# Kernel tuning notes

Hardware: AMD Instinct MI355X
Metric: run time of the kernel (lower is better)

The kernel has to match this reference:

```python
import jax, jax.numpy as jnp
import numpy as np

FACTOR = 5  # sampling factor c

def setup_inputs() -> dict:
    key = jax.random.key(0)
    k1, k2, k3, k4 = jax.random.split(key, 4)
    B, H, L, D = 4, 8, 2048, 64
    u = min(max(1, FACTOR * int(np.ceil(np.log(L)))), L)  # sample_k = 40
    return {
        "queries": jax.random.normal(k1, (B, H, L, D), jnp.float32),
        "keys": jax.random.normal(k2, (B, H, L, D), jnp.float32),
        "values": jax.random.normal(k3, (B, H, L, D), jnp.float32),
        "index_sample": jax.random.randint(k4, (L, u), 0, L, jnp.int32),
    }

def reference(queries, keys, values, index_sample):
    B, H, L_Q, D = queries.shape
    L_K = keys.shape[2]
    scale = 1.0 / np.sqrt(D)
    U_part = min(max(1, FACTOR * int(np.ceil(np.log(L_K)))), L_Q)  # n_top queries

    # --- _prob_QK: sampled scores + sparsity measure ---
    # K_sample[b,h,q,s,:] = keys[b,h,index_sample[q,s],:]  -> (B,H,L_Q,u,D)
    K_sample = keys[:, :, index_sample, :]
    QK_sample = jnp.einsum('bhqd,bhqsd->bhqs', queries, K_sample)  # (B,H,L_Q,u)
    M = QK_sample.max(-1) - QK_sample.sum(-1) / L_K                # (B,H,L_Q)
    _, index = jax.lax.top_k(M, U_part)                            # (B,H,U)

    # --- initial context: mean of V for non-selected queries ---
    context = jnp.broadcast_to(values.mean(-2, keepdims=True), (B, H, L_Q, D))

    # --- full attention for the top-U queries only ---
    Q_reduce = jnp.take_along_axis(queries, index[..., None], axis=2)   # (B,H,U,D)
    scores = jnp.einsum('bhud,bhkd->bhuk', Q_reduce, keys) * scale      # (B,H,U,L_K)
    attn = jax.nn.softmax(scores, axis=-1)
    out = jnp.einsum('bhuk,bhkd->bhud', attn, values)                   # (B,H,U,D)

    # --- scatter selected outputs back into the mean context ---
    bi = jnp.arange(B)[:, None, None]
    hi = jnp.arange(H)[None, :, None]
    context = context.at[bi, hi, index].set(out)
    return context
```

## Files before the change

### kernel.cpp

```cpp
#include <hip/hip_runtime.h>
#include <math.h>

#define Bq 4
#define Hh 8
#define Lh 2048
#define Dh 64
#define BH (Bq*Hh)

__global__ __launch_bounds__(256) void kAC(const float* __restrict__ Q,
                                           const float* __restrict__ K,
                                           const float* __restrict__ V,
                                           const int* __restrict__ idxs,
                                           float2* __restrict__ M2,
                                           float* __restrict__ vpart, int u) {
    int bi = blockIdx.x;
    int tid = threadIdx.x;
    if (bi < 2048) {
        int xcd = bi & 7, slot = bi >> 3;
        int bh  = xcd * 4 + (slot >> 6);
        int qt  = (slot >> 1) & 31;
        int half = slot & 1;
        int wave = tid >> 6, lane = tid & 63;
        int g = lane >> 2, c = lane & 3;
        int q = qt * 64 + wave * 16 + g;
        long gq = (long)bh * Lh + q;

        const float* qrow = Q + gq * Dh;
        float4 qf[4];
#pragma unroll
        for (int jj = 0; jj < 4; ++jj)
            qf[jj] = *(const float4*)(qrow + jj * 16 + c * 4);

        int cnt1 = u >> 1;
        int c0 = (half == 0) ? (u - cnt1) : cnt1;
        const int* irow = idxs + (long)q * u + (half ? (u - cnt1) : 0);
        const float* kbase = K + (long)bh * Lh * Dh;

        float mx = -INFINITY, sm = 0.f;
        int s = 0;
        for (; s + 4 <= c0; s += 4) {
            int i0 = irow[s], i1 = irow[s+1], i2 = irow[s+2], i3 = irow[s+3];
            const float* kp0 = kbase + (long)i0 * Dh + c * 4;
            const float* kp1 = kbase + (long)i1 * Dh + c * 4;
            const float* kp2 = kbase + (long)i2 * Dh + c * 4;
            const float* kp3 = kbase + (long)i3 * Dh + c * 4;
            float4 kf[4][4];
#pragma unroll
            for (int jj = 0; jj < 4; ++jj) {
                kf[0][jj] = *(const float4*)(kp0 + jj * 16);
                kf[1][jj] = *(const float4*)(kp1 + jj * 16);
                kf[2][jj] = *(const float4*)(kp2 + jj * 16);
                kf[3][jj] = *(const float4*)(kp3 + jj * 16);
            }
            float a[4];
#pragma unroll
            for (int r = 0; r < 4; ++r) {
                float ac = 0.f;
#pragma unroll
                for (int jj = 0; jj < 4; ++jj)
                    ac += qf[jj].x*kf[r][jj].x + qf[jj].y*kf[r][jj].y
                        + qf[jj].z*kf[r][jj].z + qf[jj].w*kf[r][jj].w;
                a[r] = ac;
            }
#pragma unroll
            for (int r = 0; r < 4; ++r) {
                a[r] += __shfl_xor(a[r], 1);
                a[r] += __shfl_xor(a[r], 2);
                mx = fmaxf(mx, a[r]); sm += a[r];
            }
        }
        for (; s < c0; ++s) {
            int ki = irow[s];
            const float* krow = kbase + (long)ki * Dh + c * 4;
            float acc = 0.f;
#pragma unroll
            for (int jj = 0; jj < 4; ++jj) {
                float4 kf = *(const float4*)(krow + jj * 16);
                acc += qf[jj].x*kf.x + qf[jj].y*kf.y + qf[jj].z*kf.z + qf[jj].w*kf.w;
            }
            acc += __shfl_xor(acc, 1);
            acc += __shfl_xor(acc, 2);
            mx = fmaxf(mx, acc); sm += acc;
        }
        if (c == 0) M2[gq * 2 + half] = make_float2(mx, sm);
    } else {
        int b2 = bi - 2048;
        int xcd = b2 & 7, slot = b2 >> 3;
        int bh = xcd * 4 + (slot >> 3);
        int chunk = slot & 7;
        int d = tid & 63, r0 = tid >> 6;
        const float* vb = V + ((long)bh * Lh + chunk * 256) * Dh;
        float s = 0.f;
        for (int i = 0; i < 64; ++i) s += vb[(r0 + 4 * i) * Dh + d];
        __shared__ float part[4][64];
        part[r0][d] = s;
        __syncthreads();
        if (tid < 64) {
            float t = part[0][tid] + part[1][tid] + part[2][tid] + part[3][tid];
            vpart[(bh * 8 + chunk) * 64 + tid] = t;
        }
    }
}

__global__ __launch_bounds__(256) void kBE(const float2* __restrict__ M2,
                                           const float* __restrict__ vpart,
                                           int* __restrict__ topk,
                                           float* __restrict__ ctx, int U) {
    int bi = blockIdx.x;
    int tid = threadIdx.x;
    if (bi < 4096) {
        long base = (long)bi * 1024;
        int bh = (int)(base >> 17);
        __shared__ float vm[64];
        if (tid < 64) {
            float s = 0.f;
#pragma unroll
            for (int c2 = 0; c2 < 8; ++c2) s += vpart[(bh * 8 + c2) * 64 + tid];
            vm[tid] = s * (1.0f / (float)Lh);
        }
        __syncthreads();
        float4 val = *(const float4*)(vm + ((tid * 4) & 63));
        *(float4*)(ctx + base + tid * 4) = val;
        return;
    }
    int bh = bi - 4096;
    unsigned key[8];
#pragma unroll
    for (int j = 0; j < 8; ++j) {
        long q = (long)bh * Lh + tid + 256 * j;
        float4 mm = *(const float4*)(&M2[q * 2]);
        float Mv = fmaxf(mm.x, mm.z) - (mm.y + mm.w) * (1.0f / (float)Lh);
        unsigned ub = __float_as_uint(Mv);
        key[j] = ub ^ ((ub >> 31) ? 0xFFFFFFFFu : 0x80000000u);
    }
    __shared__ unsigned hist[256];
    __shared__ unsigned prefix_s;
    __shared__ int need_s;
    if (tid == 0) { prefix_s = 0u; need_s = U; }

    for (int level = 3; level >= 0; --level) {
        int shift = level * 8;
        hist[tid] = 0u;
        __syncthreads();
        unsigned prefix = prefix_s;
        int need = need_s;
        unsigned pmask = (level == 3) ? 0u : (0xFFFFFFFFu << (shift + 8));
#pragma unroll
        for (int j = 0; j < 8; ++j)
            if ((key[j] & pmask) == prefix)
                atomicAdd(&hist[(key[j] >> shift) & 0xFF], 1u);
        __syncthreads();
        if (tid < 64) {
            int lane = tid;
            unsigned h0 = hist[lane*4+0], h1 = hist[lane*4+1],
                     h2 = hist[lane*4+2], h3 = hist[lane*4+3];
            unsigned lt = h0 + h1 + h2 + h3;
            unsigned ssum = lt;
#pragma unroll
            for (int off = 1; off < 64; off <<= 1) {
                unsigned t = __shfl_down(ssum, off);
                if (lane + off < 64) ssum += t;
            }
            unsigned sx  = ssum - lt;
            unsigned suf3 = sx  + h3;
            unsigned suf2 = suf3 + h2;
            unsigned suf1 = suf2 + h1;
            unsigned suf0 = suf1 + h0;
            int localb = -1; unsigned nxt = 0u;
            if      ((int)suf3 >= need) { localb = lane*4+3; nxt = sx;   }
            else if ((int)suf2 >= need) { localb = lane*4+2; nxt = suf3; }
            else if ((int)suf1 >= need) { localb = lane*4+1; nxt = suf2; }
            else if ((int)suf0 >= need) { localb = lane*4+0; nxt = suf1; }
            unsigned long long ball = __ballot(localb >= 0);
            int hilane = 63 - __clzll(ball);
            if (lane == hilane) {
                prefix_s = prefix | ((unsigned)localb << shift);
                need_s = need - (int)nxt;
            }
        }
        __syncthreads();
    }
    unsigned T = prefix_s;
    int r = need_s;
    __shared__ int cgt, ceq;
    if (tid == 0) { cgt = 0; ceq = 0; }
    __syncthreads();
    int* out = topk + bh * U;
#pragma unroll
    for (int j = 0; j < 8; ++j) {
        if (key[j] > T) { int p = atomicAdd(&cgt, 1); out[p] = tid + 256 * j; }
        else if (key[j] == T) { int e = atomicAdd(&ceq, 1); if (e < r) out[U - r + e] = tid + 256 * j; }
    }
}

#define TK 64
__global__ __launch_bounds__(256) void kD_part(const float* __restrict__ Q,
                                               const float* __restrict__ K,
                                               const float* __restrict__ V,
                                               const int* __restrict__ topk,
                                               float* __restrict__ pm,
                                               float* __restrict__ pl,
                                               float* __restrict__ pacc,
                                               int U, int nch) {
    int bi = blockIdx.x;
    int xcd = bi & 7, slot = bi >> 3;
    int per = nch * 8;
    int bh = xcd * 4 + slot / per;
    int rest = slot % per;
    int uc = rest >> 3, kc = rest & 7;

    int tid = threadIdx.x;
    int wv = tid >> 6, lane = tid & 63;

    __shared__ float Qs[8 * 64];
    __shared__ float Ks[TK * 68];
    __shared__ float Ps[8 * 68];
    __shared__ float alph[8], mst[8], lst[8];
    __shared__ int   qidxs[8];
    float* accbuf = Ks;

    if (tid < 8) {
        int gu = uc * 8 + tid;
        qidxs[tid] = (gu < U) ? topk[bh * U + gu] : 0;
    }
    __syncthreads();
#pragma unroll
    for (int step = 0; step < 2; ++step) {
        int uu = step * 4 + wv;
        int row = qidxs[uu];
        Qs[uu * 64 + lane] = Q[((long)bh * Lh + row) * Dh + lane] * 0.125f;
    }

    int kq = lane, ug = wv;
    float mrun0 = -INFINITY, mrun1 = -INFINITY;
    float lrun0 = 0.f, lrun1 = 0.f;
    float accv[8] = {0.f,0.f,0.f,0.f,0.f,0.f,0.f,0.f};

    const long kvbase = (long)bh * Lh * Dh;
    const float4* Kg4 = (const float4*)(K + kvbase);
    const float*  Vg  = V + kvbase;
    int kbase0 = kc * 256;

    for (int t = 0; t < 4; ++t) {
        int t0 = kbase0 + t * TK;
        int f40 = t0 * (Dh / 4);
#pragma unroll
        for (int j = 0; j < 4; ++j) {
            int i = tid + 256 * j;
            float4 kv = Kg4[f40 + i];
            int row = i >> 4, col = i & 15;
            *(float4*)(&Ks[row * 68 + col * 4]) = kv;
        }
        __syncthreads();

        float s0 = 0.f, s1 = 0.f;
#pragma unroll
        for (int j16 = 0; j16 < 16; ++j16) {
            float4 kf = *(const float4*)(&Ks[kq * 68 + j16 * 4]);
            float4 qa = *(const float4*)(&Qs[(2 * ug + 0) * 64 + j16 * 4]);
            float4 qb = *(const float4*)(&Qs[(2 * ug + 1) * 64 + j16 * 4]);
            s0 += kf.x * qa.x + kf.y * qa.y + kf.z * qa.z + kf.w * qa.w;
            s1 += kf.x * qb.x + kf.y * qb.y + kf.z * qb.z + kf.w * qb.w;
        }
        float m0 = s0, m1 = s1;
#pragma unroll
        for (int off = 1; off < 64; off <<= 1) {
            m0 = fmaxf(m0, __shfl_xor(m0, off));
            m1 = fmaxf(m1, __shfl_xor(m1, off));
        }
        float mn0 = fmaxf(mrun0, m0), mn1 = fmaxf(mrun1, m1);
        float a0 = __expf(mrun0 - mn0), a1 = __expf(mrun1 - mn1);
        float p0 = __expf(s0 - mn0),  p1 = __expf(s1 - mn1);
        float ls0 = p0, ls1 = p1;
#pragma unroll
        for (int off = 1; off < 64; off <<= 1) {
            ls0 += __shfl_xor(ls0, off);
            ls1 += __shfl_xor(ls1, off);
        }
        lrun0 = a0 * lrun0 + ls0;  lrun1 = a1 * lrun1 + ls1;
        mrun0 = mn0;               mrun1 = mn1;
        Ps[(2 * ug + 0) * 68 + kq] = p0;
        Ps[(2 * ug + 1) * 68 + kq] = p1;
        if (lane == 0) { alph[2 * ug] = a0; alph[2 * ug + 1] = a1; }
        __syncthreads();

        float vk[16];
        int vrow0 = t0 + wv * 16;
#pragma unroll
        for (int k = 0; k < 16; ++k)
            vk[k] = Vg[(long)(vrow0 + k) * Dh + lane];
#pragma unroll
        for (int u2 = 0; u2 < 8; ++u2) {
            const float* pb = &Ps[u2 * 68 + wv * 16];
            float4 pA = *(const float4*)(pb + 0);
            float4 pB = *(const float4*)(pb + 4);
            float4 pC = *(const float4*)(pb + 8);
            float4 pD = *(const float4*)(pb + 12);
            float av = alph[u2];
            float ac = accv[u2] * av;
            ac += pA.x*vk[0]  + pA.y*vk[1]  + pA.z*vk[2]  + pA.w*vk[3];
            ac += pB.x*vk[4]  + pB.y*vk[5]  + pB.z*vk[6]  + pB.w*vk[7];
            ac += pC.x*vk[8]  + pC.y*vk[9]  + pC.z*vk[10] + pC.w*vk[11];
            ac += pD.x*vk[12] + pD.y*vk[13] + pD.z*vk[14] + pD.w*vk[15];
            accv[u2] = ac;
        }
    }

    if (lane == 0) {
        mst[2 * ug] = mrun0;     lst[2 * ug] = lrun0;
        mst[2 * ug + 1] = mrun1; lst[2 * ug + 1] = lrun1;
    }
#pragma unroll
    for (int u2 = 0; u2 < 8; ++u2)
        accbuf[wv * 512 + u2 * 64 + lane] = accv[u2];
    __syncthreads();

    int pbase = (bh * nch + uc) * 8;
    {
        int d = tid & 63, ua = tid >> 6;
#pragma unroll
        for (int h = 0; h < 2; ++h) {
            int u2 = ua + 4 * h;
            float o = accbuf[0 * 512 + u2 * 64 + d] + accbuf[1 * 512 + u2 * 64 + d]
                    + accbuf[2 * 512 + u2 * 64 + d] + accbuf[3 * 512 + u2 * 64 + d];
            pacc[((long)(pbase + u2) * 8 + kc) * 64 + d] = o;
        }
    }
    if (tid < 8) {
        int qp = (pbase + tid) * 8 + kc;
        pm[qp] = mst[tid];
        pl[qp] = lst[tid];
    }
}

__global__ __launch_bounds__(256) void kF_comb(const float* __restrict__ pm,
                                               const float* __restrict__ pl,
                                               const float* __restrict__ pacc,
                                               const int* __restrict__ topk,
                                               float* __restrict__ ctx,
                                               int U, int nch) {
    int bi = blockIdx.x;
    int bh = bi / nch, uc = bi % nch;
    int tid = threadIdx.x;
    int u = tid >> 5, t = tid & 31;
    int gu = uc * 8 + u;
    if (gu >= U) return;
    int qbase = (bh * nch + uc) * 8 + u;
    float m[8], l[8];
#pragma unroll
    for (int kc = 0; kc < 8; ++kc) { m[kc] = pm[qbase * 8 + kc]; l[kc] = pl[qbase * 8 + kc]; }
    float gm = m[0];
#pragma unroll
    for (int kc = 1; kc < 8; ++kc) gm = fmaxf(gm, m[kc]);
    float w[8]; float gl = 0.f;
#pragma unroll
    for (int kc = 0; kc < 8; ++kc) { w[kc] = __expf(m[kc] - gm); gl += l[kc] * w[kc]; }
    float inv = 1.0f / gl;
    float o0 = 0.f, o1 = 0.f;
#pragma unroll
    for (int kc = 0; kc < 8; ++kc) {
        const float* a = pacc + ((long)qbase * 8 + kc) * 64;
        o0 += a[t] * w[kc];
        o1 += a[t + 32] * w[kc];
    }
    int row = topk[bh * U + gu];
    float* crow = ctx + ((long)bh * Lh + row) * Dh;
    crow[t]      = o0 * inv;
    crow[t + 32] = o1 * inv;
}

extern "C" void kernel_launch(void* const* d_in, const int* in_sizes, int n_in,
                              void* d_out, int out_size, void* d_ws, size_t ws_size,
                              hipStream_t stream) {
    const float* Q    = (const float*)d_in[0];
    const float* K    = (const float*)d_in[1];
    const float* V    = (const float*)d_in[2];
    const int*   idxs = (const int*)d_in[3];
    float* ctx = (float*)d_out;

    int u = in_sizes[3] / Lh;
    int U = u;
    int nch = (U + 7) / 8;

    float*  wsf   = (float*)d_ws;
    float2* M2    = (float2*)wsf;
    int*    topk  = (int*)(wsf + 262144);
    float*  vpart = wsf + 262144 + 2048;
    float*  pm    = wsf + 280576;
    float*  pl    = pm + 32 * nch * 8 * 8;
    float*  pacc  = pl + 32 * nch * 8 * 8;

    kAC    <<<2304,         256, 0, stream>>>(Q, K, V, idxs, M2, vpart, u);
    kBE    <<<4128,         256, 0, stream>>>(M2, vpart, topk, ctx, U);
    kD_part<<<BH * nch * 8, 256, 0, stream>>>(Q, K, V, topk, pm, pl, pacc, U, nch);
    kF_comb<<<BH * nch,     256, 0, stream>>>(pm, pl, pacc, topk, ctx, U, nch);
}
```

Measured before the change: 153.4 us.

## Double key tile size in sparse attention and prefetch sample indices as int4

The partial attention kernel now stages 128 keys per tile instead of 64. This halves the number of tile iterations, so there are half as many max/sum cross-lane reductions and barriers per block, at the cost of more shared memory (a larger K tile and P buffer). The sampled-score kernel now loads the index row four at a time as int4 and prefetches the next group one iteration ahead. This assumes each index row segment is 16-byte aligned, which may not hold when u or the half offset is not a multiple of four.

```diff
diff --git a/kernel.cpp b/kernel.cpp
--- a/kernel.cpp
+++ b/kernel.cpp
@@ -37,13 +37,18 @@
         const float* kbase = K + (long)bh * Lh * Dh;
 
         float mx = -INFINITY, sm = 0.f;
-        int s = 0;
-        for (; s + 4 <= c0; s += 4) {
-            int i0 = irow[s], i1 = irow[s+1], i2 = irow[s+2], i3 = irow[s+3];
-            const float* kp0 = kbase + (long)i0 * Dh + c * 4;
-            const float* kp1 = kbase + (long)i1 * Dh + c * 4;
-            const float* kp2 = kbase + (long)i2 * Dh + c * 4;
-            const float* kp3 = kbase + (long)i3 * Dh + c * 4;
+        int nb4 = c0 >> 2;
+        int4 ki;
+        if (nb4 > 0) ki = *(const int4*)(irow);
+        for (int b = 0; b < nb4; ++b) {
+            int4 kin;
+            bool hasn = (b + 1 < nb4);
+            if (hasn) kin = *(const int4*)(irow + 4 * (b + 1));
+
+            const float* kp0 = kbase + (long)ki.x * Dh + c * 4;
+            const float* kp1 = kbase + (long)ki.y * Dh + c * 4;
+            const float* kp2 = kbase + (long)ki.z * Dh + c * 4;
+            const float* kp3 = kbase + (long)ki.w * Dh + c * 4;
             float4 kf[4][4];
 #pragma unroll
             for (int jj = 0; jj < 4; ++jj) {
@@ -68,10 +73,11 @@
                 a[r] += __shfl_xor(a[r], 2);
                 mx = fmaxf(mx, a[r]); sm += a[r];
             }
-        }
-        for (; s < c0; ++s) {
-            int ki = irow[s];
-            const float* krow = kbase + (long)ki * Dh + c * 4;
+            if (hasn) ki = kin;
+        }
+        for (int s = nb4 * 4; s < c0; ++s) {
+            int kii = irow[s];
+            const float* krow = kbase + (long)kii * Dh + c * 4;
             float acc = 0.f;
 #pragma unroll
             for (int jj = 0; jj < 4; ++jj) {
@@ -193,7 +199,7 @@
     }
 }
 
-#define TK 64
+#define TK2 128
 __global__ __launch_bounds__(256) void kD_part(const float* __restrict__ Q,
                                                const float* __restrict__ K,
                                                const float* __restrict__ V,
@@ -213,8 +219,8 @@
     int wv = tid >> 6, lane = tid & 63;
 
     __shared__ float Qs[8 * 64];
-    __shared__ float Ks[TK * 68];
-    __shared__ float Ps[8 * 68];
+    __shared__ float Ks[TK2 * 68];
+    __shared__ float Ps[8 * 132];
     __shared__ float alph[8], mst[8], lst[8];
     __shared__ int   qidxs[8];
     float* accbuf = Ks;
@@ -241,11 +247,12 @@
     const float*  Vg  = V + kvbase;
     int kbase0 = kc * 256;
 
-    for (int t = 0; t < 4; ++t) {
-        int t0 = kbase0 + t * TK;
+#pragma unroll 1
+    for (int t = 0; t < 2; ++t) {
+        int t0 = kbase0 + t * TK2;
         int f40 = t0 * (Dh / 4);
 #pragma unroll
-        for (int j = 0; j < 4; ++j) {
+        for (int j = 0; j < 8; ++j) {
             int i = tid + 256 * j;
             float4 kv = Kg4[f40 + i];
             int row = i >> 4, col = i & 15;
@@ -253,16 +260,22 @@
         }
         __syncthreads();
 
-        float s0 = 0.f, s1 = 0.f;
-#pragma unroll
-        for (int j16 = 0; j16 < 16; ++j16) {
-            float4 kf = *(const float4*)(&Ks[kq * 68 + j16 * 4]);
-            float4 qa = *(const float4*)(&Qs[(2 * ug + 0) * 64 + j16 * 4]);
-            float4 qb = *(const float4*)(&Qs[(2 * ug + 1) * 64 + j16 * 4]);
-            s0 += kf.x * qa.x + kf.y * qa.y + kf.z * qa.z + kf.w * qa.w;
-            s1 += kf.x * qb.x + kf.y * qb.y + kf.z * qb.z + kf.w * qb.w;
-        }
-        float m0 = s0, m1 = s1;
+        float s0r[2], s1r[2];
+#pragma unroll
+        for (int rnd = 0; rnd < 2; ++rnd) {
+            int kk = rnd * 64 + kq;
+            float a0 = 0.f, a1 = 0.f;
+#pragma unroll
+            for (int j16 = 0; j16 < 16; ++j16) {
+                float4 kf = *(const float4*)(&Ks[kk * 68 + j16 * 4]);
+                float4 qa = *(const float4*)(&Qs[(2 * ug + 0) * 64 + j16 * 4]);
+                float4 qb = *(const float4*)(&Qs[(2 * ug + 1) * 64 + j16 * 4]);
+                a0 += kf.x * qa.x + kf.y * qa.y + kf.z * qa.z + kf.w * qa.w;
+                a1 += kf.x * qb.x + kf.y * qb.y + kf.z * qb.z + kf.w * qb.w;
+            }
+            s0r[rnd] = a0; s1r[rnd] = a1;
+        }
+        float m0 = fmaxf(s0r[0], s0r[1]), m1 = fmaxf(s1r[0], s1r[1]);
 #pragma unroll
         for (int off = 1; off < 64; off <<= 1) {
             m0 = fmaxf(m0, __shfl_xor(m0, off));
@@ -270,8 +283,9 @@
         }
         float mn0 = fmaxf(mrun0, m0), mn1 = fmaxf(mrun1, m1);
         float a0 = __expf(mrun0 - mn0), a1 = __expf(mrun1 - mn1);
-        float p0 = __expf(s0 - mn0),  p1 = __expf(s1 - mn1);
-        float ls0 = p0, ls1 = p1;
+        float p00 = __expf(s0r[0] - mn0), p01 = __expf(s0r[1] - mn0);
+        float p10 = __expf(s1r[0] - mn1), p11 = __expf(s1r[1] - mn1);
+        float ls0 = p00 + p01, ls1 = p10 + p11;
 #pragma unroll
         for (int off = 1; off < 64; off <<= 1) {
             ls0 += __shfl_xor(ls0, off);
@@ -279,30 +293,35 @@
         }
         lrun0 = a0 * lrun0 + ls0;  lrun1 = a1 * lrun1 + ls1;
         mrun0 = mn0;               mrun1 = mn1;
-        Ps[(2 * ug + 0) * 68 + kq] = p0;
-        Ps[(2 * ug + 1) * 68 + kq] = p1;
+        Ps[(2 * ug + 0) * 132 + kq]      = p00;
+        Ps[(2 * ug + 0) * 132 + 64 + kq] = p01;
+        Ps[(2 * ug + 1) * 132 + kq]      = p10;
+        Ps[(2 * ug + 1) * 132 + 64 + kq] = p11;
         if (lane == 0) { alph[2 * ug] = a0; alph[2 * ug + 1] = a1; }
         __syncthreads();
 
-        float vk[16];
-        int vrow0 = t0 + wv * 16;
-#pragma unroll
-        for (int k = 0; k < 16; ++k)
-            vk[k] = Vg[(long)(vrow0 + k) * Dh + lane];
-#pragma unroll
-        for (int u2 = 0; u2 < 8; ++u2) {
-            const float* pb = &Ps[u2 * 68 + wv * 16];
-            float4 pA = *(const float4*)(pb + 0);
-            float4 pB = *(const float4*)(pb + 4);
-            float4 pC = *(const float4*)(pb + 8);
-            float4 pD = *(const float4*)(pb + 12);
-            float av = alph[u2];
-            float ac = accv[u2] * av;
-            ac += pA.x*vk[0]  + pA.y*vk[1]  + pA.z*vk[2]  + pA.w*vk[3];
-            ac += pB.x*vk[4]  + pB.y*vk[5]  + pB.z*vk[6]  + pB.w*vk[7];
-            ac += pC.x*vk[8]  + pC.y*vk[9]  + pC.z*vk[10] + pC.w*vk[11];
-            ac += pD.x*vk[12] + pD.y*vk[13] + pD.z*vk[14] + pD.w*vk[15];
-            accv[u2] = ac;
+#pragma unroll 1
+        for (int h = 0; h < 2; ++h) {
+            int kb = h * 64 + wv * 16;
+            float vk[16];
+#pragma unroll
+            for (int k = 0; k < 16; ++k)
+                vk[k] = Vg[(long)(t0 + kb + k) * Dh + lane];
+#pragma unroll
+            for (int u2 = 0; u2 < 8; ++u2) {
+                const float* pb = &Ps[u2 * 132 + kb];
+                float4 pA = *(const float4*)(pb + 0);
+                float4 pB = *(const float4*)(pb + 4);
+                float4 pC = *(const float4*)(pb + 8);
+                float4 pD = *(const float4*)(pb + 12);
+                float av = (h == 0) ? alph[u2] : 1.0f;
+                float ac = accv[u2] * av;
+                ac += pA.x*vk[0]  + pA.y*vk[1]  + pA.z*vk[2]  + pA.w*vk[3];
+                ac += pB.x*vk[4]  + pB.y*vk[5]  + pB.z*vk[6]  + pB.w*vk[7];
+                ac += pC.x*vk[8]  + pC.y*vk[9]  + pC.z*vk[10] + pC.w*vk[11];
+                ac += pD.x*vk[12] + pD.y*vk[13] + pD.z*vk[14] + pD.w*vk[15];
+                accv[u2] = ac;
+            }
         }
     }
 
```

Result: slower. 158.7 us (+3.4%).
